# Kernel optimization log

Measured on AMD Instinct MI355X. Metric: run time of the kernel, lower is better.

## Reference

```python
import jax, jax.numpy as jnp
import numpy as np

T, B, C, H, W = 4, 8, 256, 56, 56
HEADS = 8
D_NORM = 8.0
LAMDA = 1
CV = C * LAMDA
EPS = 1e-5


def quant_if(x, D):
    # Q_IFNode with Quant surrogate: integer spike counts clip(round(x),0,D),
    # straight-through gradient = 1 on [0, D].
    y = jnp.clip(jnp.round(x), 0.0, D)
    mask = ((x >= 0.0) & (x <= D)).astype(x.dtype)
    return x * mask + jax.lax.stop_gradient(y - x * mask)


def conv_bn(x, w, p):
    # 1x1 conv (pointwise channel mix) fused with eval-mode BatchNorm.
    # x: [T,B,Cin,H,W], w: [Cout,Cin], p: [4,Cout]=(gamma,beta,mean,var)
    y = jnp.einsum('oc,tbchw->tbohw', w, x)
    gamma, beta, mean, var = p[0], p[1], p[2], p[3]
    s = gamma / jnp.sqrt(var + EPS)
    return y * s[None, None, :, None, None] + (beta - mean * s)[None, None, :, None, None]


def _to_heads(t, c):
    # [T,B,c,H,W] -> [T,B,HEADS,N,c//HEADS]  (channel split h-outer, matches torch reshape)
    return t.reshape(T, B, HEADS, c // HEADS, H * W).transpose(0, 1, 2, 4, 3)


def setup_inputs():
    key = jax.random.key(0)
    ks = jax.random.split(key, 9)

    def bn_params(k, c):
        k1, k2, k3, k4 = jax.random.split(k, 4)
        return jnp.stack([
            jax.random.uniform(k1, (c,)) + 0.5,        # gamma
            jax.random.normal(k2, (c,)) * 0.1,          # beta
            jax.random.normal(k3, (c,)) * 0.1,          # running mean
            jax.random.uniform(k4, (c,)) + 0.5,         # running var
        ]).astype(jnp.float32)

    x = jax.random.normal(ks[0], (T, B, C, H, W), dtype=jnp.float32)
    w_scale = 1.0 / np.sqrt(C)
    return {
        'x': x,
        'qw': jax.random.normal(ks[1], (C, C), dtype=jnp.float32) * w_scale,
        'qbn': bn_params(ks[2], C),
        'kw': jax.random.normal(ks[3], (C, C), dtype=jnp.float32) * w_scale,
        'kbn': bn_params(ks[4], C),
        'vw': jax.random.normal(ks[5], (CV, C), dtype=jnp.float32) * w_scale,
        'vbn': bn_params(ks[6], CV),
        'pw': jax.random.normal(ks[7], (C, CV), dtype=jnp.float32) * w_scale,
        'pbn': bn_params(ks[8], C),
    }


def reference(x, qw, qbn, kw, kbn, vw, vbn, pw, pbn):
    dh = C // HEADS
    scale = dh ** (-0.5)

    xs = quant_if(x, D_NORM) / D_NORM                       # head_spike / D_Norm
    q = conv_bn(xs, qw, qbn)
    k = conv_bn(xs, kw, kbn)
    v = conv_bn(xs, vw, vbn)

    qh = _to_heads(quant_if(q, D_NORM) / D_NORM, C)         # [T,B,h,N,dh]
    kh = _to_heads(quant_if(k, D_NORM) / D_NORM, C)
    vh = _to_heads(quant_if(v, D_NORM) / D_NORM, CV)        # [T,B,h,N,dv]

    # Softmax-free linear attention: (q @ k^T) @ v == q @ (k^T @ v), O(N*d^2).
    kv = jnp.einsum('tbhnd,tbhne->tbhde', kh, vh)            # [T,B,h,dh,dv]
    o = jnp.einsum('tbhnd,tbhde->tbhne', qh, kv) * (scale * 2.0)

    # [T,B,h,N,dv] -> [T,B,CV,N]
    o = o.transpose(0, 1, 2, 4, 3).reshape(T, B, CV, H * W)
    o = quant_if(o, D_NORM) / D_NORM                         # attn_spike / D_Norm
    o = o.reshape(T, B, CV, H, W)
    out = conv_bn(o, pw, pbn)                                # [T,B,C,H,W]
    return out
```

## Files before the change

### kernel.cpp

```cpp
#include <hip/hip_runtime.h>
#include <stdint.h>

#define TB_ 32
#define C_ 256
#define N_ 3136
#define TBC (C_ * N_)
#define ACT_SZ (TB_ * TBC)
#define XSB_TB 819200
#define PARTS 7
#define CHUNK 448

typedef __attribute__((ext_vector_type(8))) short bf16x8;
typedef __attribute__((ext_vector_type(4))) float f32x4;

__device__ __forceinline__ void glds16(const void* gp, void* lp) {
  __builtin_amdgcn_global_load_lds(
      (const __attribute__((address_space(1))) unsigned int*)gp,
      (__attribute__((address_space(3))) unsigned int*)lp, 16, 0, 0);
}

__device__ __forceinline__ unsigned short bf16rn(float f, float* val) {
  unsigned b = __float_as_uint(f);
  unsigned r = (b + 0x7fffu + ((b >> 16) & 1u)) >> 16;
  *val = __uint_as_float(r << 16);
  return (unsigned short)r;
}

__device__ __forceinline__ int dot4u(unsigned a, unsigned b, int c) {
  c += (int)(a & 255u)         * (int)(b & 255u);
  c += (int)((a >> 8) & 255u)  * (int)((b >> 8) & 255u);
  c += (int)((a >> 16) & 255u) * (int)((b >> 16) & 255u);
  c += (int)(a >> 24)          * (int)(b >> 24);
  return c;
}

__device__ __forceinline__ int dot4(unsigned a, unsigned b, int c) {
#if defined(__has_builtin)
#if __has_builtin(__builtin_amdgcn_sdot4)
  return __builtin_amdgcn_sdot4((int)a, (int)b, c, false);
#else
  return dot4u(a, b, c);
#endif
#else
  return dot4u(a, b, c);
#endif
}

__global__ __launch_bounds__(256) void prep_all(
    const float* __restrict__ qbn, const float* __restrict__ kbn,
    const float* __restrict__ vbn, const float* __restrict__ pbn,
    const float* __restrict__ qw, const float* __restrict__ kw,
    const float* __restrict__ vw, const float* __restrict__ pw,
    float* __restrict__ bnw, unsigned short* __restrict__ wsp,
    int* __restrict__ kvg) {
  const int bx = blockIdx.x;
  const int t = threadIdx.x;
  if (bx == 0) {
    const float* ps[4] = {qbn, kbn, vbn, pbn};
#pragma unroll
    for (int i = 0; i < 4; ++i) {
      const float* p = ps[i];
      float g = p[t], be = p[256 + t], mn = p[512 + t], vr = p[768 + t];
      float s = g / sqrtf(vr + 1e-5f);
      float b = __fsub_rn(be, __fmul_rn(mn, s));
      bnw[i * 512 + t] = s;
      bnw[i * 512 + 256 + t] = b;
    }
  } else if (bx <= 1024) {
    const float* Ws[4] = {qw, kw, vw, pw};
    int id = bx - 1, co = id & 255, m = id >> 8;
    float w = Ws[m][co * 256 + t];
    float h1, h2, h3r;
    unsigned short u1 = bf16rn(w, &h1);
    float r1 = __fsub_rn(w, h1);
    unsigned short u2 = bf16rn(r1, &h2);
    float r2 = __fsub_rn(r1, h2);
    unsigned short u3 = bf16rn(r2, &h3r);
    int rt = co >> 7, ks = t >> 5;
    int lane = (co & 15) + 16 * ((t >> 3) & 3);
    unsigned short us[3] = {u1, u2, u3};
#pragma unroll
    for (int sp = 0; sp < 3; ++sp) {
      size_t off = (size_t)((((m * 3 + sp) * 2 + rt) * 8 + ks)) * 4096 + lane * 8 + (t & 7);
      wsp[off] = us[sp];
    }
  } else {
    int tb = bx - 1025;
    int4* p = (int4*)(kvg + (size_t)tb * 8192);
    for (int i = t; i < 2048; i += 256) p[i] = make_int4(0, 0, 0, 0);
  }
}

__global__ __launch_bounds__(256) void quant_x_t(const float* __restrict__ x,
                                                 unsigned short* __restrict__ xsb) {
  __shared__ unsigned short s[64 * 68];
  const int t = threadIdx.x;
  const int n0 = blockIdx.x * 64;
  const int tb = blockIdx.y;
  const float* X = x + (size_t)tb * TBC;
  const int nl = t & 63, cq = t >> 6;
  const int c16 = t >> 4, p4 = (t & 15) * 4;

  unsigned short* dstb = xsb + (size_t)tb * XSB_TB;
  for (int cb = 0; cb < 4; ++cb) {
    int cbase = cb * 64;
#pragma unroll
    for (int i = 0; i < 4; ++i) {
      int c = i * 16 + c16;
      float4 v = *(const float4*)&X[(size_t)(cbase + c) * N_ + n0 + p4];
      unsigned short r0 = (unsigned short)(__float_as_uint(fminf(fmaxf(rintf(v.x), 0.f), 8.f)) >> 16);
      unsigned short r1 = (unsigned short)(__float_as_uint(fminf(fmaxf(rintf(v.y), 0.f), 8.f)) >> 16);
      unsigned short r2 = (unsigned short)(__float_as_uint(fminf(fmaxf(rintf(v.z), 0.f), 8.f)) >> 16);
      unsigned short r3 = (unsigned short)(__float_as_uint(fminf(fmaxf(rintf(v.w), 0.f), 8.f)) >> 16);
      uint2 pk2;
      pk2.x = (unsigned)r0 | ((unsigned)r1 << 16);
      pk2.y = (unsigned)r2 | ((unsigned)r3 << 16);
      *(uint2*)&s[c * 68 + p4] = pk2;
    }
    __syncthreads();
#pragma unroll 2
    for (int j = 0; j < 2; ++j) {
      int ccl = j * 4 + cq;
      int cc = cb * 8 + ccl;
      unsigned short v8[8];
#pragma unroll
      for (int d = 0; d < 8; ++d) v8[d] = s[(ccl * 8 + d) * 68 + nl];
      int n = n0 + nl;
      uint4 pk;
      pk.x = (unsigned)v8[0] | ((unsigned)v8[1] << 16);
      pk.y = (unsigned)v8[2] | ((unsigned)v8[3] << 16);
      pk.z = (unsigned)v8[4] | ((unsigned)v8[5] << 16);
      pk.w = (unsigned)v8[6] | ((unsigned)v8[7] << 16);
      *(uint4*)&dstb[(size_t)(n >> 4) * 4096 + cc * 128 + (n & 15) * 8] = pk;
    }
    __syncthreads();
  }
}

__global__ __launch_bounds__(256) void qkv_mfma_sw(
    const unsigned short* __restrict__ xsb, const unsigned short* __restrict__ wsp,
    const float* __restrict__ bnw,
    uint8_t* __restrict__ qsb, uint8_t* __restrict__ ks_, uint8_t* __restrict__ vs) {
  __shared__ __align__(16) char smem[49152];
  const int t = threadIdx.x;
  const int L = t & 63, w = t >> 6;
  const int wrow = w >> 1, wcol = w & 1;
  const int b = blockIdx.x;
  const int oct = b / 48, rem = b % 48;
  const int s = rem >> 3, gl = rem & 7;
  const int g = oct * 8 + gl;
  const int ntile = g % 25, tb = g / 25;
  const int conv = s >> 1, rt = s & 1;
  const int n0 = ntile * 128;

  const char* Bb = (const char*)(xsb + (size_t)tb * XSB_TB) + (size_t)ntile * 65536;
  const char* Ab = (const char*)wsp + ((size_t)(conv * 3) * 16 + rt * 8) * 8192;

  f32x4 acc[4][4];
#pragma unroll
  for (int i = 0; i < 4; ++i)
#pragma unroll
    for (int j = 0; j < 4; ++j) acc[i][j] = (f32x4){0.f, 0.f, 0.f, 0.f};

  glds16(Ab + t * 16, smem + t * 16);
  glds16(Ab + t * 16 + 4096, smem + t * 16 + 4096);
  glds16(Bb + (size_t)w * 8192 + L * 16, smem + 8192 + t * 16);
  glds16(Bb + (size_t)(w + 4) * 8192 + L * 16, smem + 8192 + t * 16 + 4096);

#pragma unroll 1
  for (int st = 0; st < 24; ++st) {
    char* slotc = smem + (st % 3) * 16384;
    if (st < 23) {
      const int s1 = st + 1;
      char* slotn = smem + (s1 % 3) * 16384;
      const char* Ak = Ab + (size_t)(((s1 >> 3) * 16) + (s1 & 7)) * 8192;
      glds16(Ak + t * 16, slotn + t * 16);
      glds16(Ak + t * 16 + 4096, slotn + t * 16 + 4096);
      const char* Bk = Bb + (size_t)(s1 & 7) * 1024;
      glds16(Bk + (size_t)w * 8192 + L * 16, slotn + 8192 + t * 16);
      glds16(Bk + (size_t)(w + 4) * 8192 + L * 16, slotn + 8192 + t * 16 + 4096);
      asm volatile("s_waitcnt vmcnt(4)" ::: "memory");
    } else {
      asm volatile("s_waitcnt vmcnt(0)" ::: "memory");
    }
    __builtin_amdgcn_s_barrier();
    bf16x8 af[4], bfr[4];
#pragma unroll
    for (int i = 0; i < 4; ++i) {
      af[i] = *(const bf16x8*)(slotc + (wrow * 4 + i) * 1024 + L * 16);
      bfr[i] = *(const bf16x8*)(slotc + 8192 + (wcol * 4 + i) * 1024 + L * 16);
    }
#pragma unroll
    for (int i = 0; i < 4; ++i)
#pragma unroll
      for (int j = 0; j < 4; ++j)
        acc[i][j] = __builtin_amdgcn_mfma_f32_16x16x32_bf16(af[i], bfr[j], acc[i][j], 0, 0, 0);
  }

  const float* sbn = bnw + conv * 512;
  const int rbase = rt * 128;
  if (conv == 0) {
    uint8_t* qtb = qsb + (size_t)tb * XSB_TB;
#pragma unroll
    for (int i = 0; i < 4; ++i) {
      int co0 = rbase + wrow * 64 + i * 16 + ((L >> 4) << 2);
      float s0 = sbn[co0], b0 = sbn[256 + co0];
      float s1 = sbn[co0 + 1], b1 = sbn[256 + co0 + 1];
      float s2 = sbn[co0 + 2], b2 = sbn[256 + co0 + 2];
      float s3 = sbn[co0 + 3], b3 = sbn[256 + co0 + 3];
#pragma unroll
      for (int j = 0; j < 4; ++j) {
        int n = n0 + wcol * 64 + j * 16 + (L & 15);
        if (n < N_) {
          float ss[4] = {s0, s1, s2, s3}, bb[4] = {b0, b1, b2, b3};
          unsigned wb = 0;
#pragma unroll
          for (int r = 0; r < 4; ++r) {
            float y = acc[i][j][r] * 0.125f;
            float tt = __fadd_rn(__fmul_rn(y, ss[r]), bb[r]);
            float rr = fminf(fmaxf(rintf(tt), 0.f), 8.f);
            wb |= ((unsigned)(uint8_t)rr) << (8 * r);
          }
          *(unsigned*)&qtb[(size_t)(n >> 4) * 4096 + (co0 >> 3) * 128 + (n & 15) * 8 + (co0 & 7)] = wb;
        }
      }
    }
  } else {
    uint8_t* outp = (conv == 1 ? ks_ : vs) + (size_t)tb * TBC;
#pragma unroll
    for (int i = 0; i < 4; ++i) {
      int co0 = rbase + wrow * 64 + i * 16 + ((L >> 4) << 2);
#pragma unroll
      for (int j = 0; j < 4; ++j) {
        int n = n0 + wcol * 64 + j * 16 + (L & 15);
        if (n < N_) {
#pragma unroll
          for (int r = 0; r < 4; ++r) {
            int co = co0 + r;
            float y = acc[i][j][r] * 0.125f;
            float tt = __fadd_rn(__fmul_rn(y, sbn[co]), sbn[256 + co]);
            float rr = fminf(fmaxf(rintf(tt), 0.f), 8.f);
            outp[(size_t)co * N_ + n] = (uint8_t)rr;
          }
        }
      }
    }
  }
}

__global__ __launch_bounds__(256) void attn_kv(
    const uint8_t* __restrict__ ks, const uint8_t* __restrict__ vs,
    int* __restrict__ kvg) {
  const int h = blockIdx.x, tb = blockIdx.y, part = blockIdx.z;
  const int tid = threadIdx.x;
  __shared__ unsigned sk[32][68];
  __shared__ unsigned sv[32][68];
  const uint8_t* K = ks + (size_t)tb * TBC + h * 32 * N_;
  const uint8_t* V = vs + (size_t)tb * TBC + h * 32 * N_;
  const int d0 = (tid >> 4) * 2;
  const int e0 = (tid & 15) * 2;
  const int pbase = part * CHUNK;
  const int pend = pbase + CHUNK;
  int acc[2][2] = {};

  for (int nt = 0; nt < 2; ++nt) {
    int n0 = pbase + nt * 256;
    if (n0 >= pend) break;
    if (nt) __syncthreads();
#pragma unroll
    for (int i = 0; i < 8; ++i) {
      int idx = tid + i * 256;
      int d = idx >> 6, w2 = idx & 63;
      int n = n0 + w2 * 4;
      unsigned kw_ = 0, vw_ = 0;
      if (n < pend) {
        kw_ = *(const unsigned*)&K[d * N_ + n];
        vw_ = *(const unsigned*)&V[d * N_ + n];
      }
      sk[d][w2] = kw_;
      sv[d][w2] = vw_;
    }
    __syncthreads();
#pragma unroll
    for (int w2 = 0; w2 < 64; w2 += 4) {
      uint4 ka = *(const uint4*)&sk[d0][w2];
      uint4 kb = *(const uint4*)&sk[d0 + 1][w2];
      uint4 va = *(const uint4*)&sv[e0][w2];
      uint4 vb = *(const uint4*)&sv[e0 + 1][w2];
      unsigned kwds[2][4] = {{ka.x, ka.y, ka.z, ka.w}, {kb.x, kb.y, kb.z, kb.w}};
      unsigned vwds[2][4] = {{va.x, va.y, va.z, va.w}, {vb.x, vb.y, vb.z, vb.w}};
#pragma unroll
      for (int di = 0; di < 2; ++di)
#pragma unroll
        for (int ej = 0; ej < 2; ++ej)
#pragma unroll
          for (int c = 0; c < 4; ++c)
            acc[di][ej] = dot4(kwds[di][c], vwds[ej][c], acc[di][ej]);
    }
  }
  int* dst = kvg + ((size_t)(tb * 8 + h)) * 1024;
  atomicAdd(&dst[d0 * 32 + e0], acc[0][0]);
  atomicAdd(&dst[d0 * 32 + e0 + 1], acc[0][1]);
  atomicAdd(&dst[(d0 + 1) * 32 + e0], acc[1][0]);
  atomicAdd(&dst[(d0 + 1) * 32 + e0 + 1], acc[1][1]);
}

__global__ __launch_bounds__(256) void kv_finish(const int* __restrict__ kvg,
                                                 unsigned short* __restrict__ kvimg) {
  const int tb = blockIdx.x, t = threadIdx.x;
  const int* src = kvg + (size_t)tb * 8192;
  unsigned short* dst = kvimg + (size_t)tb * 24576;
#pragma unroll 4
  for (int i = 0; i < 32; ++i) {
    int idx = t + i * 256;
    int h = idx >> 10, rem = idx & 1023, d = rem >> 5, e = rem & 31;
    int v = src[idx];
    int b1 = (v > 0) ? (32 - __clz(v)) : 0;
    int sh1 = b1 > 8 ? b1 - 8 : 0;
    int hi = (v >> sh1) << sh1;
    int r1 = v - hi;
    int b2 = (r1 > 0) ? (32 - __clz(r1)) : 0;
    int sh2 = b2 > 8 ? b2 - 8 : 0;
    int mid = (r1 >> sh2) << sh2;
    int r2 = r1 - mid;
    int parts[3] = {hi, mid, r2};
    int mtile = e >> 4, lane = (e & 15) + 16 * (d >> 3), j = d & 7;
#pragma unroll
    for (int sp = 0; sp < 3; ++sp) {
      float f = (float)parts[sp];
      dst[(size_t)h * 3072 + (sp * 2 + mtile) * 512 + lane * 8 + j] =
          (unsigned short)(__float_as_uint(f) >> 16);
    }
  }
}

__global__ __launch_bounds__(256) void attn_o_mfma(
    const uint8_t* __restrict__ qsb, const unsigned short* __restrict__ kvimg,
    unsigned short* __restrict__ osb) {
  __shared__ __align__(16) char smem[14336];
  char* smB = smem;
  char* smA = smem + 8192;
  const int t = threadIdx.x;
  const int L = t & 63, wv = t >> 6;
  const int b = blockIdx.x;
  const int ntile = b % 25, tb = b / 25;
  const uint8_t* Q = qsb + (size_t)tb * XSB_TB + (size_t)ntile * 8 * 4096;
  const unsigned short* KV = kvimg + (size_t)tb * 24576;
  unsigned short* osb_tb = osb + (size_t)tb * XSB_TB;
  const float cscale = (float)(0.3535533905932738 / 512.0);

#pragma unroll 1
  for (int h = 0; h < 8; ++h) {
    __syncthreads();
    const char* Ah = (const char*)(KV + (size_t)h * 3072);
    glds16(Ah + t * 16, smA + t * 16);
    if (t < 128) glds16(Ah + 4096 + t * 16, smA + 4096 + t * 16);
#pragma unroll
    for (int it = 0; it < 4; ++it) {
      int w2 = t + it * 256;
      int gl2 = w2 >> 7;
      int wl = w2 & 127;
      int ccp = wl >> 5;
      int rem = (w2 * 4) & 127;
      int n16 = rem >> 3, k7b = rem & 7;
      unsigned wd = *(const unsigned*)&Q[(size_t)gl2 * 4096 + (h * 4 + ccp) * 128 + n16 * 8 + k7b];
      unsigned short* ds = (unsigned short*)smB + gl2 * 512 + (ccp * 16 + n16) * 8 + k7b;
      float f0 = (float)(wd & 255u), f1 = (float)((wd >> 8) & 255u);
      float f2 = (float)((wd >> 16) & 255u), f3 = (float)(wd >> 24);
      uint2 pk;
      pk.x = (__float_as_uint(f0) >> 16) | ((__float_as_uint(f1) >> 16) << 16);
      pk.y = (__float_as_uint(f2) >> 16) | ((__float_as_uint(f3) >> 16) << 16);
      *(uint2*)ds = pk;
    }
    __syncthreads();
    bf16x8 bfr[2];
#pragma unroll
    for (int jj = 0; jj < 2; ++jj)
      bfr[jj] = *(const bf16x8*)(smB + (wv * 2 + jj) * 1024 + L * 16);
    f32x4 acc[2][2];
#pragma unroll
    for (int i = 0; i < 2; ++i)
#pragma unroll
      for (int jj = 0; jj < 2; ++jj) acc[i][jj] = (f32x4){0.f, 0.f, 0.f, 0.f};
#pragma unroll
    for (int sp = 0; sp < 3; ++sp) {
      bf16x8 a0 = *(const bf16x8*)(smA + (sp * 2 + 0) * 1024 + L * 16);
      bf16x8 a1 = *(const bf16x8*)(smA + (sp * 2 + 1) * 1024 + L * 16);
#pragma unroll
      for (int jj = 0; jj < 2; ++jj) {
        acc[0][jj] = __builtin_amdgcn_mfma_f32_16x16x32_bf16(a0, bfr[jj], acc[0][jj], 0, 0, 0);
        acc[1][jj] = __builtin_amdgcn_mfma_f32_16x16x32_bf16(a1, bfr[jj], acc[1][jj], 0, 0, 0);
      }
    }
#pragma unroll
    for (int i = 0; i < 2; ++i) {
      int c0 = h * 32 + i * 16 + ((L >> 4) << 2);
#pragma unroll
      for (int jj = 0; jj < 2; ++jj) {
        int n = ntile * 128 + (wv * 2 + jj) * 16 + (L & 15);
        if (n < N_) {
          unsigned short u[4];
#pragma unroll
          for (int r = 0; r < 4; ++r) {
            float of = acc[i][jj][r] * cscale;
            float rr = fminf(fmaxf(rintf(of), 0.f), 8.f);
            u[r] = (unsigned short)(__float_as_uint(rr) >> 16);
          }
          uint2 pk;
          pk.x = (unsigned)u[0] | ((unsigned)u[1] << 16);
          pk.y = (unsigned)u[2] | ((unsigned)u[3] << 16);
          *(uint2*)&osb_tb[(size_t)(n >> 4) * 4096 + (c0 >> 3) * 128 + (n & 15) * 8 + (c0 & 7)] = pk;
        }
      }
    }
  }
}

__global__ __launch_bounds__(256) void out_mfma_sw(
    const unsigned short* __restrict__ osb, const unsigned short* __restrict__ wsp,
    const float* __restrict__ bnw, float* __restrict__ out) {
  __shared__ __align__(16) char smem[49152];
  const int t = threadIdx.x;
  const int L = t & 63, w = t >> 6;
  const int wrow = w >> 1, wcol = w & 1;
  const int b = blockIdx.x;
  const int oct = b / 16, rem = b % 16;
  const int rt = rem >> 3, gl = rem & 7;
  const int g = oct * 8 + gl;
  const int ntile = g % 25, tb = g / 25;
  const int n0 = ntile * 128;
  const char* Bb = (const char*)(osb + (size_t)tb * XSB_TB) + (size_t)ntile * 65536;
  const char* Ab = (const char*)wsp + ((size_t)9 * 16 + rt * 8) * 8192;

  f32x4 acc[4][4];
#pragma unroll
  for (int i = 0; i < 4; ++i)
#pragma unroll
    for (int j = 0; j < 4; ++j) acc[i][j] = (f32x4){0.f, 0.f, 0.f, 0.f};

  glds16(Ab + t * 16, smem + t * 16);
  glds16(Ab + t * 16 + 4096, smem + t * 16 + 4096);
  glds16(Bb + (size_t)w * 8192 + L * 16, smem + 8192 + t * 16);
  glds16(Bb + (size_t)(w + 4) * 8192 + L * 16, smem + 8192 + t * 16 + 4096);

#pragma unroll 1
  for (int st = 0; st < 16; ++st) {
    char* slotc = smem + (st % 3) * 16384;
    if (st < 15) {
      const int s1 = st + 1;
      char* slotn = smem + (s1 % 3) * 16384;
      const char* Ak = Ab + (size_t)(((s1 >> 3) * 16) + (s1 & 7)) * 8192;
      glds16(Ak + t * 16, slotn + t * 16);
      glds16(Ak + t * 16 + 4096, slotn + t * 16 + 4096);
      const char* Bk = Bb + (size_t)(s1 & 7) * 1024;
      glds16(Bk + (size_t)w * 8192 + L * 16, slotn + 8192 + t * 16);
      glds16(Bk + (size_t)(w + 4) * 8192 + L * 16, slotn + 8192 + t * 16 + 4096);
      asm volatile("s_waitcnt vmcnt(4)" ::: "memory");
    } else {
      asm volatile("s_waitcnt vmcnt(0)" ::: "memory");
    }
    __builtin_amdgcn_s_barrier();
    bf16x8 af[4], bfr[4];
#pragma unroll
    for (int i = 0; i < 4; ++i) {
      af[i] = *(const bf16x8*)(slotc + (wrow * 4 + i) * 1024 + L * 16);
      bfr[i] = *(const bf16x8*)(slotc + 8192 + (wcol * 4 + i) * 1024 + L * 16);
    }
#pragma unroll
    for (int i = 0; i < 4; ++i)
#pragma unroll
      for (int j = 0; j < 4; ++j)
        acc[i][j] = __builtin_amdgcn_mfma_f32_16x16x32_bf16(af[i], bfr[j], acc[i][j], 0, 0, 0);
  }

  float* O = out + (size_t)tb * TBC;
  const float* sbn = bnw + 3 * 512;
  const int rbase = rt * 128;
#pragma unroll
  for (int i = 0; i < 4; ++i) {
    int co0 = rbase + wrow * 64 + i * 16 + ((L >> 4) << 2);
#pragma unroll
    for (int j = 0; j < 4; ++j) {
      int n = n0 + wcol * 64 + j * 16 + (L & 15);
      if (n < N_) {
#pragma unroll
        for (int r = 0; r < 4; ++r) {
          int co = co0 + r;
          float y = acc[i][j][r] * 0.125f;
          O[(size_t)co * N_ + n] = __fadd_rn(__fmul_rn(y, sbn[co]), sbn[256 + co]);
        }
      }
    }
  }
}

extern "C" void kernel_launch(void* const* d_in, const int* in_sizes, int n_in,
                              void* d_out, int out_size, void* d_ws, size_t ws_size,
                              hipStream_t stream) {
  const float* x   = (const float*)d_in[0];
  const float* qw  = (const float*)d_in[1];
  const float* qbn = (const float*)d_in[2];
  const float* kw  = (const float*)d_in[3];
  const float* kbn = (const float*)d_in[4];
  const float* vw  = (const float*)d_in[5];
  const float* vbn = (const float*)d_in[6];
  const float* pw  = (const float*)d_in[7];
  const float* pbn = (const float*)d_in[8];
  float* out = (float*)d_out;

  uint8_t* ws = (uint8_t*)d_ws;
  float* bnw           = (float*)ws;
  unsigned short* wsp  = (unsigned short*)(ws + 8192);
  unsigned short* xsb  = (unsigned short*)(ws + 1581056);
  uint8_t* qsb         = ws + 54009856;
  uint8_t* ksp         = ws + 80224256;
  uint8_t* vsp         = ws + 105914368;
  int* kvg             = (int*)(ws + 131604480);
  unsigned short* kvimg = (unsigned short*)(ws + 132653056);
  unsigned short* osb  = xsb;

  prep_all<<<1057, 256, 0, stream>>>(qbn, kbn, vbn, pbn, qw, kw, vw, pw, bnw, wsp, kvg);
  quant_x_t<<<dim3(49, 32), 256, 0, stream>>>(x, xsb);
  qkv_mfma_sw<<<4800, 256, 0, stream>>>(xsb, wsp, bnw, qsb, ksp, vsp);
  attn_kv<<<dim3(8, 32, PARTS), 256, 0, stream>>>(ksp, vsp, kvg);
  kv_finish<<<32, 256, 0, stream>>>(kvg, kvimg);
  attn_o_mfma<<<800, 256, 0, stream>>>(qsb, kvimg, osb);
  out_mfma_sw<<<1600, 256, 0, stream>>>(osb, wsp, bnw, out);
}
```

Baseline: 394.7 us.

## Enlarge GEMM block tiles to full 256 output channels and swizzle attn_kv LDS

The qkv and output projection GEMM kernels now compute all 256 output channels per block (each wave covers 64 rows by 128 columns) instead of splitting rows across two blocks. This halves the grid and reuses each activation tile for twice as many outputs. The pipeline changes from a 3-slot buffer with vmcnt(4) to a 2-slot double buffer that waits for all loads each step, which may expose more load latency. The attn_kv kernel also XOR-swizzles the V tile in LDS to reduce bank conflicts. Register use rises to 128 accumulator floats per thread, which can lower occupancy.

```diff
diff --git a/kernel.cpp b/kernel.cpp
--- a/kernel.cpp
+++ b/kernel.cpp
@@ -144,75 +144,80 @@
   __shared__ __align__(16) char smem[49152];
   const int t = threadIdx.x;
   const int L = t & 63, w = t >> 6;
-  const int wrow = w >> 1, wcol = w & 1;
   const int b = blockIdx.x;
-  const int oct = b / 48, rem = b % 48;
-  const int s = rem >> 3, gl = rem & 7;
+  const int oct = b / 24, rem = b % 24;
+  const int conv = rem >> 3, gl = rem & 7;
   const int g = oct * 8 + gl;
   const int ntile = g % 25, tb = g / 25;
-  const int conv = s >> 1, rt = s & 1;
   const int n0 = ntile * 128;
 
   const char* Bb = (const char*)(xsb + (size_t)tb * XSB_TB) + (size_t)ntile * 65536;
-  const char* Ab = (const char*)wsp + ((size_t)(conv * 3) * 16 + rt * 8) * 8192;
-
-  f32x4 acc[4][4];
+  const char* Ab = (const char*)wsp + (size_t)(conv * 3 * 16) * 8192;
+
+  f32x4 acc[4][8];
 #pragma unroll
   for (int i = 0; i < 4; ++i)
 #pragma unroll
-    for (int j = 0; j < 4; ++j) acc[i][j] = (f32x4){0.f, 0.f, 0.f, 0.f};
-
-  glds16(Ab + t * 16, smem + t * 16);
-  glds16(Ab + t * 16 + 4096, smem + t * 16 + 4096);
-  glds16(Bb + (size_t)w * 8192 + L * 16, smem + 8192 + t * 16);
-  glds16(Bb + (size_t)(w + 4) * 8192 + L * 16, smem + 8192 + t * 16 + 4096);
+    for (int j = 0; j < 8; ++j) acc[i][j] = (f32x4){0.f, 0.f, 0.f, 0.f};
+
+  {
+    const char* Ak0 = Ab;
+    const char* Ak1 = Ab + (size_t)8 * 8192;
+    glds16(Ak0 + t * 16, smem + t * 16);
+    glds16(Ak0 + t * 16 + 4096, smem + t * 16 + 4096);
+    glds16(Ak1 + t * 16, smem + 8192 + t * 16);
+    glds16(Ak1 + t * 16 + 4096, smem + 8192 + t * 16 + 4096);
+    glds16(Bb + (size_t)w * 8192 + L * 16, smem + 16384 + t * 16);
+    glds16(Bb + (size_t)(w + 4) * 8192 + L * 16, smem + 16384 + t * 16 + 4096);
+  }
 
 #pragma unroll 1
   for (int st = 0; st < 24; ++st) {
-    char* slotc = smem + (st % 3) * 16384;
-    if (st < 23) {
-      const int s1 = st + 1;
-      char* slotn = smem + (s1 % 3) * 16384;
-      const char* Ak = Ab + (size_t)(((s1 >> 3) * 16) + (s1 & 7)) * 8192;
-      glds16(Ak + t * 16, slotn + t * 16);
-      glds16(Ak + t * 16 + 4096, slotn + t * 16 + 4096);
+    asm volatile("s_waitcnt vmcnt(0)" ::: "memory");
+    __builtin_amdgcn_s_barrier();
+    const int s1 = st + 1;
+    if (s1 < 24) {
+      char* slotn = smem + (s1 & 1) * 24576;
+      const int slab = ((s1 >> 3) * 16) + (s1 & 7);
+      const char* Ak0 = Ab + (size_t)slab * 8192;
+      const char* Ak1 = Ab + (size_t)(slab + 8) * 8192;
+      glds16(Ak0 + t * 16, slotn + t * 16);
+      glds16(Ak0 + t * 16 + 4096, slotn + t * 16 + 4096);
+      glds16(Ak1 + t * 16, slotn + 8192 + t * 16);
+      glds16(Ak1 + t * 16 + 4096, slotn + 8192 + t * 16 + 4096);
       const char* Bk = Bb + (size_t)(s1 & 7) * 1024;
-      glds16(Bk + (size_t)w * 8192 + L * 16, slotn + 8192 + t * 16);
-      glds16(Bk + (size_t)(w + 4) * 8192 + L * 16, slotn + 8192 + t * 16 + 4096);
-      asm volatile("s_waitcnt vmcnt(4)" ::: "memory");
-    } else {
-      asm volatile("s_waitcnt vmcnt(0)" ::: "memory");
-    }
-    __builtin_amdgcn_s_barrier();
-    bf16x8 af[4], bfr[4];
-#pragma unroll
-    for (int i = 0; i < 4; ++i) {
-      af[i] = *(const bf16x8*)(slotc + (wrow * 4 + i) * 1024 + L * 16);
-      bfr[i] = *(const bf16x8*)(slotc + 8192 + (wcol * 4 + i) * 1024 + L * 16);
-    }
-#pragma unroll
-    for (int i = 0; i < 4; ++i)
-#pragma unroll
-      for (int j = 0; j < 4; ++j)
-        acc[i][j] = __builtin_amdgcn_mfma_f32_16x16x32_bf16(af[i], bfr[j], acc[i][j], 0, 0, 0);
+      glds16(Bk + (size_t)w * 8192 + L * 16, slotn + 16384 + t * 16);
+      glds16(Bk + (size_t)(w + 4) * 8192 + L * 16, slotn + 16384 + t * 16 + 4096);
+    }
+    char* slotc = smem + (st & 1) * 24576;
+    const char* aw = slotc + (w >> 1) * 8192 + (w & 1) * 4096;
+    bf16x8 af[4];
+#pragma unroll
+    for (int i = 0; i < 4; ++i) af[i] = *(const bf16x8*)(aw + i * 1024 + L * 16);
+#pragma unroll
+    for (int j = 0; j < 8; ++j) {
+      bf16x8 bfr = *(const bf16x8*)(slotc + 16384 + j * 1024 + L * 16);
+#pragma unroll
+      for (int i = 0; i < 4; ++i)
+        acc[i][j] = __builtin_amdgcn_mfma_f32_16x16x32_bf16(af[i], bfr, acc[i][j], 0, 0, 0);
+    }
   }
 
   const float* sbn = bnw + conv * 512;
-  const int rbase = rt * 128;
   if (conv == 0) {
     uint8_t* qtb = qsb + (size_t)tb * XSB_TB;
 #pragma unroll
     for (int i = 0; i < 4; ++i) {
-      int co0 = rbase + wrow * 64 + i * 16 + ((L >> 4) << 2);
+      int co0 = w * 64 + i * 16 + ((L >> 4) << 2);
       float s0 = sbn[co0], b0 = sbn[256 + co0];
       float s1 = sbn[co0 + 1], b1 = sbn[256 + co0 + 1];
-      float s2 = sbn[co0 + 2], b2 = sbn[256 + co0 + 2];
+      float s2v = sbn[co0 + 2], b2 = sbn[256 + co0 + 2];
       float s3 = sbn[co0 + 3], b3 = sbn[256 + co0 + 3];
 #pragma unroll
-      for (int j = 0; j < 4; ++j) {
-        int n = n0 + wcol * 64 + j * 16 + (L & 15);
+      for (int j = 0; j < 8; ++j) {
+        int n = n0 + j * 16 + (L & 15);
         if (n < N_) {
-          float ss[4] = {s0, s1, s2, s3}, bb[4] = {b0, b1, b2, b3};
+          float ss[4] = {s0, s1, s2v, s3}, bb[4] = {b0, b1, b2, b3};
           unsigned wb = 0;
 #pragma unroll
           for (int r = 0; r < 4; ++r) {
@@ -229,10 +234,10 @@
     uint8_t* outp = (conv == 1 ? ks_ : vs) + (size_t)tb * TBC;
 #pragma unroll
     for (int i = 0; i < 4; ++i) {
-      int co0 = rbase + wrow * 64 + i * 16 + ((L >> 4) << 2);
-#pragma unroll
-      for (int j = 0; j < 4; ++j) {
-        int n = n0 + wcol * 64 + j * 16 + (L & 15);
+      int co0 = w * 64 + i * 16 + ((L >> 4) << 2);
+#pragma unroll
+      for (int j = 0; j < 8; ++j) {
+        int n = n0 + j * 16 + (L & 15);
         if (n < N_) {
 #pragma unroll
           for (int r = 0; r < 4; ++r) {
@@ -259,6 +264,7 @@
   const uint8_t* V = vs + (size_t)tb * TBC + h * 32 * N_;
   const int d0 = (tid >> 4) * 2;
   const int e0 = (tid & 15) * 2;
+  const int vsw = ((e0 >> 1) & 7) << 2;
   const int pbase = part * CHUNK;
   const int pend = pbase + CHUNK;
   int acc[2][2] = {};
@@ -278,15 +284,15 @@
         vw_ = *(const unsigned*)&V[d * N_ + n];
       }
       sk[d][w2] = kw_;
-      sv[d][w2] = vw_;
+      sv[d][w2 ^ (((d >> 1) & 7) << 2)] = vw_;
     }
     __syncthreads();
 #pragma unroll
     for (int w2 = 0; w2 < 64; w2 += 4) {
       uint4 ka = *(const uint4*)&sk[d0][w2];
       uint4 kb = *(const uint4*)&sk[d0 + 1][w2];
-      uint4 va = *(const uint4*)&sv[e0][w2];
-      uint4 vb = *(const uint4*)&sv[e0 + 1][w2];
+      uint4 va = *(const uint4*)&sv[e0][w2 ^ vsw];
+      uint4 vb = *(const uint4*)&sv[e0 + 1][w2 ^ vsw];
       unsigned kwds[2][4] = {{ka.x, ka.y, ka.z, ka.w}, {kb.x, kb.y, kb.z, kb.w}};
       unsigned vwds[2][4] = {{va.x, va.y, va.z, va.w}, {vb.x, vb.y, vb.z, vb.w}};
 #pragma unroll
@@ -422,66 +428,69 @@
   __shared__ __align__(16) char smem[49152];
   const int t = threadIdx.x;
   const int L = t & 63, w = t >> 6;
-  const int wrow = w >> 1, wcol = w & 1;
   const int b = blockIdx.x;
-  const int oct = b / 16, rem = b % 16;
-  const int rt = rem >> 3, gl = rem & 7;
-  const int g = oct * 8 + gl;
-  const int ntile = g % 25, tb = g / 25;
+  const int ntile = b % 25, tb = b / 25;
   const int n0 = ntile * 128;
   const char* Bb = (const char*)(osb + (size_t)tb * XSB_TB) + (size_t)ntile * 65536;
-  const char* Ab = (const char*)wsp + ((size_t)9 * 16 + rt * 8) * 8192;
-
-  f32x4 acc[4][4];
+  const char* Ab = (const char*)wsp + (size_t)(9 * 16) * 8192;
+
+  f32x4 acc[4][8];
 #pragma unroll
   for (int i = 0; i < 4; ++i)
 #pragma unroll
-    for (int j = 0; j < 4; ++j) acc[i][j] = (f32x4){0.f, 0.f, 0.f, 0.f};
-
-  glds16(Ab + t * 16, smem + t * 16);
-  glds16(Ab + t * 16 + 4096, smem + t * 16 + 4096);
-  glds16(Bb + (size_t)w * 8192 + L * 16, smem + 8192 + t * 16);
-  glds16(Bb + (size_t)(w + 4) * 8192 + L * 16, smem + 8192 + t * 16 + 4096);
+    for (int j = 0; j < 8; ++j) acc[i][j] = (f32x4){0.f, 0.f, 0.f, 0.f};
+
+  {
+    const char* Ak0 = Ab;
+    const char* Ak1 = Ab + (size_t)8 * 8192;
+    glds16(Ak0 + t * 16, smem + t * 16);
+    glds16(Ak0 + t * 16 + 4096, smem + t * 16 + 4096);
+    glds16(Ak1 + t * 16, smem + 8192 + t * 16);
+    glds16(Ak1 + t * 16 + 4096, smem + 8192 + t * 16 + 4096);
+    glds16(Bb + (size_t)w * 8192 + L * 16, smem + 16384 + t * 16);
+    glds16(Bb + (size_t)(w + 4) * 8192 + L * 16, smem + 16384 + t * 16 + 4096);
+  }
 
 #pragma unroll 1
   for (int st = 0; st < 16; ++st) {
-    char* slotc = smem + (st % 3) * 16384;
-    if (st < 15) {
-      const int s1 = st + 1;
-      char* slotn = smem + (s1 % 3) * 16384;
-      const char* Ak = Ab + (size_t)(((s1 >> 3) * 16) + (s1 & 7)) * 8192;
-      glds16(Ak + t * 16, slotn + t * 16);
-      glds16(Ak + t * 16 + 4096, slotn + t * 16 + 4096);
+    asm volatile("s_waitcnt vmcnt(0)" ::: "memory");
+    __builtin_amdgcn_s_barrier();
+    const int s1 = st + 1;
+    if (s1 < 16) {
+      char* slotn = smem + (s1 & 1) * 24576;
+      const int slab = ((s1 >> 3) * 16) + (s1 & 7);
+      const char* Ak0 = Ab + (size_t)slab * 8192;
+      const char* Ak1 = Ab + (size_t)(slab + 8) * 8192;
+      glds16(Ak0 + t * 16, slotn + t * 16);
+      glds16(Ak0 + t * 16 + 4096, slotn + t * 16 + 4096);
+      glds16(Ak1 + t * 16, slotn + 8192 + t * 16);
+      glds16(Ak1 + t * 16 + 4096, slotn + 8192 + t * 16 + 4096);
       const char* Bk = Bb + (size_t)(s1 & 7) * 1024;
-      glds16(Bk + (size_t)w * 8192 + L * 16, slotn + 8192 + t * 16);
-      glds16(Bk + (size_t)(w + 4) * 8192 + L * 16, slotn + 8192 + t * 16 + 4096);
-      asm volatile("s_waitcnt vmcnt(4)" ::: "memory");
-    } else {
-      asm volatile("s_waitcnt vmcnt(0)" ::: "memory");
-    }
-    __builtin_amdgcn_s_barrier();
-    bf16x8 af[4], bfr[4];
-#pragma unroll
-    for (int i = 0; i < 4; ++i) {
-      af[i] = *(const bf16x8*)(slotc + (wrow * 4 + i) * 1024 + L * 16);
-      bfr[i] = *(const bf16x8*)(slotc + 8192 + (wcol * 4 + i) * 1024 + L * 16);
-    }
-#pragma unroll
-    for (int i = 0; i < 4; ++i)
-#pragma unroll
-      for (int j = 0; j < 4; ++j)
-        acc[i][j] = __builtin_amdgcn_mfma_f32_16x16x32_bf16(af[i], bfr[j], acc[i][j], 0, 0, 0);
+      glds16(Bk + (size_t)w * 8192 + L * 16, slotn + 16384 + t * 16);
+      glds16(Bk + (size_t)(w + 4) * 8192 + L * 16, slotn + 16384 + t * 16 + 4096);
+    }
+    char* slotc = smem + (st & 1) * 24576;
+    const char* aw = slotc + (w >> 1) * 8192 + (w & 1) * 4096;
+    bf16x8 af[4];
+#pragma unroll
+    for (int i = 0; i < 4; ++i) af[i] = *(const bf16x8*)(aw + i * 1024 + L * 16);
+#pragma unroll
+    for (int j = 0; j < 8; ++j) {
+      bf16x8 bfr = *(const bf16x8*)(slotc + 16384 + j * 1024 + L * 16);
+#pragma unroll
+      for (int i = 0; i < 4; ++i)
+        acc[i][j] = __builtin_amdgcn_mfma_f32_16x16x32_bf16(af[i], bfr, acc[i][j], 0, 0, 0);
+    }
   }
 
   float* O = out + (size_t)tb * TBC;
   const float* sbn = bnw + 3 * 512;
-  const int rbase = rt * 128;
 #pragma unroll
   for (int i = 0; i < 4; ++i) {
-    int co0 = rbase + wrow * 64 + i * 16 + ((L >> 4) << 2);
-#pragma unroll
-    for (int j = 0; j < 4; ++j) {
-      int n = n0 + wcol * 64 + j * 16 + (L & 15);
+    int co0 = w * 64 + i * 16 + ((L >> 4) << 2);
+#pragma unroll
+    for (int j = 0; j < 8; ++j) {
+      int n = n0 + j * 16 + (L & 15);
       if (n < N_) {
 #pragma unroll
         for (int r = 0; r < 4; ++r) {
@@ -521,9 +530,9 @@
 
   prep_all<<<1057, 256, 0, stream>>>(qbn, kbn, vbn, pbn, qw, kw, vw, pw, bnw, wsp, kvg);
   quant_x_t<<<dim3(49, 32), 256, 0, stream>>>(x, xsb);
-  qkv_mfma_sw<<<4800, 256, 0, stream>>>(xsb, wsp, bnw, qsb, ksp, vsp);
+  qkv_mfma_sw<<<2400, 256, 0, stream>>>(xsb, wsp, bnw, qsb, ksp, vsp);
   attn_kv<<<dim3(8, 32, PARTS), 256, 0, stream>>>(ksp, vsp, kvg);
   kv_finish<<<32, 256, 0, stream>>>(kvg, kvimg);
   attn_o_mfma<<<800, 256, 0, stream>>>(qsb, kvimg, osb);
-  out_mfma_sw<<<1600, 256, 0, stream>>>(osb, wsp, bnw, out);
-}
+  out_mfma_sw<<<800, 256, 0, stream>>>(osb, wsp, bnw, out);
+}
```

Result: slower. 525.1 us (+33.1%).
